# Kernel optimization log

Measured on AMD Instinct MI355X. Metric: run time of the kernel, lower is better.

## Reference

```python
import jax, jax.numpy as jnp
import numpy as np
import math

L, D, H, FF, V, S = 6, 512, 8, 2048, 32000, 1024
DH = D // H
EPS = 1e-5

def _ln(x, w, b):
    mu = jnp.mean(x, -1, keepdims=True)
    var = jnp.mean(jnp.square(x - mu), -1, keepdims=True)
    return (x - mu) * jax.lax.rsqrt(var + EPS) * w + b

def setup_inputs() -> dict:
    key = jax.random.key(0)
    ks = jax.random.split(key, 32)
    s = 0.02
    inp = {
        'x': jax.random.randint(ks[0], (4, S), 0, V, dtype=jnp.int32),
        'mask': jnp.ones((4, S), dtype=jnp.int32),
        'emb': jax.random.normal(ks[1], (V, D), jnp.float32) * s,
        'pos': jax.random.normal(ks[2], (S, D), jnp.float32) * s,
        'Wq': jax.random.normal(ks[3], (L, D, D), jnp.float32) * s,
        'bq': jnp.zeros((L, D), jnp.float32),
        'Wk': jax.random.normal(ks[4], (L, D, D), jnp.float32) * s,
        'bk': jnp.zeros((L, D), jnp.float32),
        'Wv': jax.random.normal(ks[5], (L, D, D), jnp.float32) * s,
        'bv': jnp.zeros((L, D), jnp.float32),
        'Wo': jax.random.normal(ks[6], (L, D, D), jnp.float32) * s,
        'bo': jnp.zeros((L, D), jnp.float32),
        'rel_bias': jax.random.normal(ks[7], (L, 2 * S - 1, H), jnp.float32) * s,
        'scale': jnp.full((L,), math.sqrt(DH), jnp.float32),
        'n1w': jnp.ones((L, D), jnp.float32), 'n1b': jnp.zeros((L, D), jnp.float32),
        'n2w': jnp.ones((L, D), jnp.float32), 'n2b': jnp.zeros((L, D), jnp.float32),
        'f1w': jax.random.normal(ks[8], (L, D, FF), jnp.float32) * s,
        'f1b': jnp.zeros((L, FF), jnp.float32),
        'f2w': jax.random.normal(ks[9], (L, FF, D), jnp.float32) * s,
        'f2b': jnp.zeros((L, D), jnp.float32),
        'fnw': jnp.ones((D,), jnp.float32), 'fnb': jnp.zeros((D,), jnp.float32),
        'fcw': jax.random.normal(ks[10], (D, V), jnp.float32) * s,
        'fcb': jnp.zeros((V,), jnp.float32),
    }
    return inp

def reference(x, mask, emb, pos, Wq, bq, Wk, bk, Wv, bv, Wo, bo, rel_bias, scale,
              n1w, n1b, n2w, n2b, f1w, f1b, f2w, f2b, fnw, fnb, fcw, fcb):
    B, seq = x.shape
    h = emb[x] * jnp.float32(math.sqrt(D)) + pos[None, :seq, :]
    # relative position index table: j - i + seq - 1, values in [0, 2*seq-2]
    r = jnp.arange(seq)
    rp = r[None, :] - r[:, None] + seq - 1  # (S, S)
    # pairwise valid mask (b,1,S,S)
    m2 = (mask[:, None, None, :] * mask[:, None, :, None]) != 0
    for l in range(L):
        q = (h @ Wq[l] + bq[l]).reshape(B, seq, H, DH)
        k = (h @ Wk[l] + bk[l]).reshape(B, seq, H, DH)
        v = (h @ Wv[l] + bv[l]).reshape(B, seq, H, DH)
        scores = jnp.einsum('bihd,bjhd->bhij', q, k) / scale[l]
        bias = rel_bias[l][rp]                      # (S,S,H)
        scores = scores + jnp.transpose(bias, (2, 0, 1))[None]
        scores = jnp.where(m2, scores, -jnp.inf)    # masked_fill(mask==0, -inf)
        attn = jnp.einsum('bhij,bjhd->bihd', scores, v).reshape(B, seq, D)
        attn = attn @ Wo[l] + bo[l]
        h = _ln(h + attn, n1w[l], n1b[l])
        ff = jax.nn.gelu(h @ f1w[l] + f1b[l], approximate=False) @ f2w[l] + f2b[l]
        h = _ln(h + ff, n2w[l], n2b[l])
    h = _ln(h, fnw, fnb)
    return h @ fcw + fcb
```

## Files before the change

### kernel.cpp

```cpp
#include <hip/hip_runtime.h>
#include <cmath>

#define S_LEN  1024
#define DMODEL 512
#define NHEAD  8
#define DHEAD  64
#define FFDIM  2048
#define VOCAB  32000
#define NLAYER 6
#define BATCHN 4
#define ROWS   (BATCHN * S_LEN)

typedef float    f32x4 __attribute__((ext_vector_type(4)));
typedef _Float16 f16x4 __attribute__((ext_vector_type(4)));
typedef _Float16 f16x8 __attribute__((ext_vector_type(8)));

__device__ __forceinline__ void glds16(const _Float16* g, _Float16* l) {
    __builtin_amdgcn_global_load_lds(
        (const __attribute__((address_space(1))) void*)g,
        (__attribute__((address_space(3))) void*)l, 16, 0, 0);
}

template<int MT, int NT, int EPI, int OUT16>
__global__ __launch_bounds__(256)
void hgemm_k(const _Float16* __restrict__ A, long lda,
             const _Float16* __restrict__ Bt, long ldb,
             void* __restrict__ Cg, long ldc, int K,
             const float* __restrict__ bias)
{
    constexpr int BMt = 32 * MT, BNt = 32 * NT;
    constexpr int ASZ = BMt * 64, BSZ = BNt * 64;
    __shared__ _Float16 As[2 * ASZ];
    __shared__ _Float16 Bs[2 * BSZ];

    const int t = threadIdx.x, w = t >> 6, lane = t & 63;
    const int m0 = blockIdx.x * BMt, n0 = blockIdx.y * BNt;
    const int lr = lane & 15, hk = lane >> 4;
    const int rsw = lr & 7;
    const int swz = ((lane & 7) ^ (lane >> 3)) * 8;

    const _Float16* Ab = A  + (long)(m0 + w * 8 * MT + (lane >> 3)) * lda + swz;
    const _Float16* Bb = Bt + (long)(n0 + w * 8 * NT + (lane >> 3)) * ldb + swz;

    f32x4 acc[MT][NT];
#pragma unroll
    for (int i = 0; i < MT; i++)
#pragma unroll
        for (int j = 0; j < NT; j++) acc[i][j] = f32x4{0.f, 0.f, 0.f, 0.f};

    const int wrow = (w >> 1) * 16 * MT;
    const int wcol = (w & 1) * 16 * NT;

    auto stage = [&](int buf, int kt) {
#pragma unroll
        for (int i = 0; i < MT; i++)
            glds16(Ab + (long)i * 8 * lda + kt, &As[buf * ASZ + (w * 8 * MT + i * 8) * 64]);
#pragma unroll
        for (int i = 0; i < NT; i++)
            glds16(Bb + (long)i * 8 * ldb + kt, &Bs[buf * BSZ + (w * 8 * NT + i * 8) * 64]);
    };

    stage(0, 0);
    __syncthreads();
    int cur = 0;
    for (int kt = 0; kt < K; kt += 64) {
        if (kt + 64 < K) stage(cur ^ 1, kt + 64);
#pragma unroll
        for (int kc = 0; kc < 64; kc += 32) {
            const int coff = ((((kc >> 3) + hk) ^ rsw) << 3);
            f16x8 af[MT], bf[NT];
#pragma unroll
            for (int mi = 0; mi < MT; mi++)
                af[mi] = *(const f16x8*)&As[cur * ASZ + (wrow + mi * 16 + lr) * 64 + coff];
#pragma unroll
            for (int ni = 0; ni < NT; ni++)
                bf[ni] = *(const f16x8*)&Bs[cur * BSZ + (wcol + ni * 16 + lr) * 64 + coff];
#pragma unroll
            for (int mi = 0; mi < MT; mi++)
#pragma unroll
                for (int ni = 0; ni < NT; ni++)
                    acc[mi][ni] = __builtin_amdgcn_mfma_f32_16x16x32_f16(af[mi], bf[ni], acc[mi][ni], 0, 0, 0);
        }
        __syncthreads();
        cur ^= 1;
    }

    const int crow = (lane >> 4) * 4, ccol = lane & 15;
#pragma unroll
    for (int mi = 0; mi < MT; mi++)
#pragma unroll
        for (int ni = 0; ni < NT; ni++)
#pragma unroll
            for (int q = 0; q < 4; q++) {
                int gm = m0 + wrow + mi * 16 + crow + q;
                int gn = n0 + wcol + ni * 16 + ccol;
                float v = acc[mi][ni][q];
                if (bias) v += bias[gn];
                if (EPI == 2) v = 0.5f * v * (1.0f + erff(v * 0.70710678118654752f));
                long ci = (long)gm * ldc + gn;
                if (OUT16) ((_Float16*)Cg)[ci] = (_Float16)v;
                else       ((float*)Cg)[ci] = v;
            }
}

__global__ __launch_bounds__(256)
void ktv_k(const _Float16* __restrict__ kt, const _Float16* __restrict__ vt,
           _Float16* __restrict__ M, const float* __restrict__ scale_p)
{
    const int z = blockIdx.x;
    const int wave = threadIdx.x >> 6, lane = threadIdx.x & 63;
    const int lr = lane & 15, lk = (lane >> 4) * 8;
    const long base = (long)z * DHEAD * S_LEN;

    f32x4 acc[4];
#pragma unroll
    for (int i = 0; i < 4; i++) acc[i] = f32x4{0.f, 0.f, 0.f, 0.f};

    for (int j = 0; j < S_LEN; j += 32) {
        f16x8 a = *(const f16x8*)&vt[base + (long)(wave * 16 + lr) * S_LEN + j + lk];
#pragma unroll
        for (int ni = 0; ni < 4; ni++) {
            f16x8 b = *(const f16x8*)&kt[base + (long)(ni * 16 + lr) * S_LEN + j + lk];
            acc[ni] = __builtin_amdgcn_mfma_f32_16x16x32_f16(a, b, acc[ni], 0, 0, 0);
        }
    }

    const float inv = 1.0f / scale_p[0];
    const int crow = (lane >> 4) * 4, ccol = lane & 15;
#pragma unroll
    for (int ni = 0; ni < 4; ni++)
#pragma unroll
        for (int q = 0; q < 4; q++) {
            int gm = wave * 16 + crow + q;
            int gn = ni * 16 + ccol;
            M[(long)z * 4096 + (long)gm * 64 + gn] = (_Float16)(acc[ni][q] * inv);
        }
}

__global__ __launch_bounds__(256)
void toep_k(const _Float16* __restrict__ dv,
            const _Float16* __restrict__ vt,
            const _Float16* __restrict__ q,
            const _Float16* __restrict__ M,
            _Float16* __restrict__ ao)
{
    __shared__ _Float16 Qs[64 * 64];
    __shared__ _Float16 Ms[64 * 64];
    __shared__ _Float16 Vs[2][64 * 64];
    __shared__ _Float16 dseg[1088];

    const int t = threadIdx.x, w = t >> 6, lane = t & 63;
    const int z = blockIdx.z, zb = z >> 3, zh = z & 7;
    const int m0 = blockIdx.x * 64;
    const int lr = lane & 15, hk = lane >> 4;
    const int rsw = lr & 7;
    const int swz = ((lane & 7) ^ (lane >> 3)) * 8;
    const int wrow = w * 16;

    const _Float16* qa = q  + (long)(zb * S_LEN + m0 + w * 16 + (lane >> 3)) * 1536 + zh * 64 + swz;
    const _Float16* ma = M  + (long)z * 4096 + (long)(w * 16 + (lane >> 3)) * 64 + swz;
    const _Float16* va = vt + (long)z * (DHEAD * S_LEN) + (long)(w * 16 + (lane >> 3)) * S_LEN + swz;

#pragma unroll
    for (int i = 0; i < 2; i++) glds16(qa + (long)i * 8 * 1536, &Qs[(w * 16 + i * 8) * 64]);
#pragma unroll
    for (int i = 0; i < 2; i++) glds16(ma + i * 8 * 64, &Ms[(w * 16 + i * 8) * 64]);
#pragma unroll
    for (int i = 0; i < 2; i++) glds16(va + (long)i * 8 * S_LEN, &Vs[0][(w * 16 + i * 8) * 64]);
    {
        const _Float16* dp = dv + zh * 2048 + (960 - m0);
        for (int i = t; i < 1088; i += 256) dseg[i] = dp[i];
    }
    __syncthreads();

    f32x4 acc[4];
#pragma unroll
    for (int i = 0; i < 4; i++) acc[i] = f32x4{0.f, 0.f, 0.f, 0.f};

#pragma unroll
    for (int kc = 0; kc < 64; kc += 32) {
        const int coff = ((((kc >> 3) + hk) ^ rsw) << 3);
        f16x8 aq = *(const f16x8*)&Qs[(wrow + lr) * 64 + coff];
#pragma unroll
        for (int ni = 0; ni < 4; ni++) {
            f16x8 bm = *(const f16x8*)&Ms[(ni * 16 + lr) * 64 + coff];
            acc[ni] = __builtin_amdgcn_mfma_f32_16x16x32_f16(aq, bm, acc[ni], 0, 0, 0);
        }
    }

    int cur = 0;
    for (int kt = 0; kt < S_LEN; kt += 64) {
        if (kt + 64 < S_LEN) {
#pragma unroll
            for (int i = 0; i < 2; i++)
                glds16(va + (long)i * 8 * S_LEN + kt + 64, &Vs[cur ^ 1][(w * 16 + i * 8) * 64]);
        }
#pragma unroll
        for (int kc = 0; kc < 64; kc += 32) {
            const int coff = ((((kc >> 3) + hk) ^ rsw) << 3);
            f16x8 at_;
            const int xb = kt + kc + hk * 8 + 63 - wrow - lr;
#pragma unroll
            for (int u = 0; u < 8; u++) at_[u] = dseg[xb + u];
#pragma unroll
            for (int ni = 0; ni < 4; ni++) {
                f16x8 bv_ = *(const f16x8*)&Vs[cur][(ni * 16 + lr) * 64 + coff];
                acc[ni] = __builtin_amdgcn_mfma_f32_16x16x32_f16(at_, bv_, acc[ni], 0, 0, 0);
            }
        }
        __syncthreads();
        cur ^= 1;
    }

    const int crow = (lane >> 4) * 4, ccol = lane & 15;
    const long cbase = (long)zb * (S_LEN * DMODEL) + zh * DHEAD;
#pragma unroll
    for (int ni = 0; ni < 4; ni++)
#pragma unroll
        for (int qq = 0; qq < 4; qq++) {
            int gm = m0 + wrow + crow + qq;
            int gn = ni * 16 + ccol;
            ao[cbase + (long)gm * DMODEL + gn] = (_Float16)acc[ni][qq];
        }
}

__global__ void embed_k(const int* __restrict__ x, const float* __restrict__ emb,
                        const float* __restrict__ pos, float* __restrict__ h,
                        _Float16* __restrict__ h16)
{
    int row = blockIdx.x;
    int s   = row & (S_LEN - 1);
    int tok = x[row];
    int c   = threadIdx.x * 4;
    f32x4 e = *(const f32x4*)(emb + (long)tok * DMODEL + c);
    f32x4 p = *(const f32x4*)(pos + (long)s * DMODEL + c);
    f32x4 o = e * 22.62741699796952f + p;
    *(f32x4*)(h + (long)row * DMODEL + c) = o;
    f16x4 o16;
#pragma unroll
    for (int j = 0; j < 4; j++) o16[j] = (_Float16)o[j];
    *(f16x4*)(h16 + (long)row * DMODEL + c) = o16;
}

__global__ void ln_k(const float* __restrict__ x, const float* __restrict__ add,
                     const float* __restrict__ w, const float* __restrict__ bb,
                     float* __restrict__ out, _Float16* __restrict__ out16)
{
    int row  = blockIdx.x;
    int lane = threadIdx.x;
    const float* xp = x + (long)row * DMODEL + lane * 8;
    f32x4 a = *(const f32x4*)xp;
    f32x4 b4 = *(const f32x4*)(xp + 4);
    if (add) {
        const float* ap = add + (long)row * DMODEL + lane * 8;
        a  += *(const f32x4*)ap;
        b4 += *(const f32x4*)(ap + 4);
    }
    float v[8] = {a[0],a[1],a[2],a[3],b4[0],b4[1],b4[2],b4[3]};
    float s = 0.f;
#pragma unroll
    for (int i = 0; i < 8; i++) s += v[i];
#pragma unroll
    for (int off = 32; off; off >>= 1) s += __shfl_xor(s, off);
    float mu = s * (1.0f / 512.0f);
    float d2 = 0.f;
#pragma unroll
    for (int i = 0; i < 8; i++) { v[i] -= mu; d2 += v[i] * v[i]; }
#pragma unroll
    for (int off = 32; off; off >>= 1) d2 += __shfl_xor(d2, off);
    float r = rsqrtf(d2 * (1.0f / 512.0f) + 1e-5f);
    const float* wp = w  + lane * 8;
    const float* bp = bb + lane * 8;
    float o[8];
#pragma unroll
    for (int i = 0; i < 8; i++) o[i] = v[i] * r * wp[i] + bp[i];
    float* op = out + (long)row * DMODEL + lane * 8;
    *(f32x4*)op       = f32x4{o[0], o[1], o[2], o[3]};
    *(f32x4*)(op + 4) = f32x4{o[4], o[5], o[6], o[7]};
    f16x8 o16;
#pragma unroll
    for (int i = 0; i < 8; i++) o16[i] = (_Float16)o[i];
    *(f16x8*)(out16 + (long)row * DMODEL + lane * 8) = o16;
}

__global__ void wcvt_k(const float* __restrict__ in, _Float16* __restrict__ out,
                       int R, int C, long inZ, long outZ)
{
    __shared__ float tile[32][33];
    int z = blockIdx.z;
    int c0 = blockIdx.x * 32, r0 = blockIdx.y * 32;
    int tx = threadIdx.x, ty = threadIdx.y;
#pragma unroll
    for (int i = 0; i < 4; i++)
        tile[ty + i * 8][tx] = in[(long)z * inZ + (long)(r0 + ty + i * 8) * C + c0 + tx];
    __syncthreads();
#pragma unroll
    for (int i = 0; i < 4; i++)
        out[(long)z * outZ + (long)(c0 + ty + i * 8) * R + r0 + tx] = (_Float16)tile[tx][ty + i * 8];
}

__global__ void tv16_k(const _Float16* __restrict__ v, long ldv, _Float16* __restrict__ vt)
{
    __shared__ _Float16 tile[32][33];
    int z = blockIdx.z;
    int b = z >> 3, hh = z & 7;
    int j0 = blockIdx.x * 32, d0 = blockIdx.y * 32;
    long ibase = (long)b * S_LEN * ldv + hh * DHEAD;
    long obase = (long)z * (DHEAD * S_LEN);
    int tx = threadIdx.x, ty = threadIdx.y;
#pragma unroll
    for (int i = 0; i < 4; i++)
        tile[ty + i * 8][tx] = v[ibase + (long)(j0 + ty + i * 8) * ldv + d0 + tx];
    __syncthreads();
#pragma unroll
    for (int i = 0; i < 4; i++)
        vt[obase + (long)(d0 + ty + i * 8) * S_LEN + j0 + tx] = tile[tx][ty + i * 8];
}

__global__ void bcat_k(const float* __restrict__ bq, const float* __restrict__ bk,
                       const float* __restrict__ bv, float* __restrict__ o)
{
    int l = blockIdx.x, t = threadIdx.x;
    o[l * 1536 + t]        = bq[l * 512 + t];
    o[l * 1536 + 512 + t]  = bk[l * 512 + t];
    o[l * 1536 + 1024 + t] = bv[l * 512 + t];
}

__global__ void dvec_k(const float* __restrict__ rel, _Float16* __restrict__ dv)
{
    int lh = blockIdx.x;
    int l = lh >> 3, hh = lh & 7;
    for (int t = threadIdx.x; t < 2048; t += 256)
        dv[(long)lh * 2048 + t] = (t < 2047) ? (_Float16)rel[(long)l * 2047 * 8 + (long)t * 8 + hh]
                                             : (_Float16)0.0f;
}

extern "C" void kernel_launch(void* const* d_in, const int* in_sizes, int n_in,
                              void* d_out, int out_size, void* d_ws, size_t ws_size,
                              hipStream_t stream)
{
    (void)in_sizes; (void)n_in; (void)out_size; (void)ws_size;

    const int*   x    = (const int*)d_in[0];
    const float* emb  = (const float*)d_in[2];
    const float* pos  = (const float*)d_in[3];
    const float* Wq   = (const float*)d_in[4];
    const float* bq   = (const float*)d_in[5];
    const float* Wk   = (const float*)d_in[6];
    const float* bk   = (const float*)d_in[7];
    const float* Wv   = (const float*)d_in[8];
    const float* bv   = (const float*)d_in[9];
    const float* Wo   = (const float*)d_in[10];
    const float* bo   = (const float*)d_in[11];
    const float* rel  = (const float*)d_in[12];
    const float* scal = (const float*)d_in[13];
    const float* n1w  = (const float*)d_in[14];
    const float* n1b  = (const float*)d_in[15];
    const float* n2w  = (const float*)d_in[16];
    const float* n2b  = (const float*)d_in[17];
    const float* f1w  = (const float*)d_in[18];
    const float* f1b  = (const float*)d_in[19];
    const float* f2w  = (const float*)d_in[20];
    const float* f2b  = (const float*)d_in[21];
    const float* fnw  = (const float*)d_in[22];
    const float* fnb  = (const float*)d_in[23];
    const float* fcw  = (const float*)d_in[24];
    const float* fcb  = (const float*)d_in[25];

    char* ws = (char*)d_ws;
    size_t off = 0;
    auto alloc = [&](size_t bytes) { char* p = ws + off; off += (bytes + 255) & ~(size_t)255; return p; };
    float*    h      = (float*)alloc((size_t)ROWS * DMODEL * 4);
    float*    proj   = (float*)alloc((size_t)ROWS * DMODEL * 4);
    float*    ff2    = (float*)alloc((size_t)ROWS * DMODEL * 4);
    _Float16* h16    = (_Float16*)alloc((size_t)ROWS * DMODEL * 2);
    _Float16* qkv16  = (_Float16*)alloc((size_t)ROWS * 3 * DMODEL * 2);
    _Float16* kt16   = (_Float16*)alloc((size_t)ROWS * DMODEL * 2);
    _Float16* vt16   = (_Float16*)alloc((size_t)ROWS * DMODEL * 2);
    _Float16* ao16   = (_Float16*)alloc((size_t)ROWS * DMODEL * 2);
    _Float16* ff116  = (_Float16*)alloc((size_t)ROWS * FFDIM * 2);
    _Float16* M16    = (_Float16*)alloc((size_t)32 * 4096 * 2);
    _Float16* wqkvT  = (_Float16*)alloc((size_t)NLAYER * 3 * DMODEL * DMODEL * 2);
    _Float16* woT    = (_Float16*)alloc((size_t)NLAYER * DMODEL * DMODEL * 2);
    _Float16* f1T    = (_Float16*)alloc((size_t)NLAYER * DMODEL * FFDIM * 2);
    _Float16* f2T    = (_Float16*)alloc((size_t)NLAYER * DMODEL * FFDIM * 2);
    _Float16* fcT    = (_Float16*)alloc((size_t)VOCAB * DMODEL * 2);
    float*    bqkv   = (float*)alloc((size_t)NLAYER * 3 * DMODEL * 4);
    _Float16* dv16   = (_Float16*)alloc((size_t)NLAYER * NHEAD * 2048 * 2);

    dim3 b256(256), bT(32, 8);

    wcvt_k<<<dim3(16, 16, NLAYER), bT, 0, stream>>>(Wq, wqkvT,               DMODEL, DMODEL, (long)DMODEL*DMODEL, (long)3*DMODEL*DMODEL);
    wcvt_k<<<dim3(16, 16, NLAYER), bT, 0, stream>>>(Wk, wqkvT + 512*512,     DMODEL, DMODEL, (long)DMODEL*DMODEL, (long)3*DMODEL*DMODEL);
    wcvt_k<<<dim3(16, 16, NLAYER), bT, 0, stream>>>(Wv, wqkvT + 2*512*512,   DMODEL, DMODEL, (long)DMODEL*DMODEL, (long)3*DMODEL*DMODEL);
    wcvt_k<<<dim3(16, 16, NLAYER), bT, 0, stream>>>(Wo, woT,                 DMODEL, DMODEL, (long)DMODEL*DMODEL, (long)DMODEL*DMODEL);
    wcvt_k<<<dim3(FFDIM/32, 16, NLAYER), bT, 0, stream>>>(f1w, f1T,          DMODEL, FFDIM,  (long)DMODEL*FFDIM,  (long)DMODEL*FFDIM);
    wcvt_k<<<dim3(16, FFDIM/32, NLAYER), bT, 0, stream>>>(f2w, f2T,          FFDIM,  DMODEL, (long)DMODEL*FFDIM,  (long)DMODEL*FFDIM);
    wcvt_k<<<dim3(VOCAB/32, 16, 1), bT, 0, stream>>>(fcw, fcT,               DMODEL, VOCAB,  0, 0);
    bcat_k<<<NLAYER, 512, 0, stream>>>(bq, bk, bv, bqkv);
    dvec_k<<<NLAYER * NHEAD, 256, 0, stream>>>(rel, dv16);

    embed_k<<<ROWS, 128, 0, stream>>>(x, emb, pos, h, h16);

    for (int l = 0; l < NLAYER; l++) {
        const long lw  = (long)l * DMODEL * DMODEL;
        const long lff = (long)l * DMODEL * FFDIM;

        hgemm_k<2,4,0,1><<<dim3(64, 12), b256, 0, stream>>>(
            h16, DMODEL, wqkvT + l * 3 * 512 * 512, DMODEL,
            qkv16, 3 * DMODEL, DMODEL, bqkv + l * 3 * DMODEL);

        tv16_k<<<dim3(32, 2, 32), bT, 0, stream>>>(qkv16 + 512,  3 * DMODEL, kt16);
        tv16_k<<<dim3(32, 2, 32), bT, 0, stream>>>(qkv16 + 1024, 3 * DMODEL, vt16);

        ktv_k<<<32, b256, 0, stream>>>(kt16, vt16, M16, scal + l);

        toep_k<<<dim3(16, 1, 32), b256, 0, stream>>>(
            dv16 + (long)l * NHEAD * 2048, vt16, qkv16, M16, ao16);

        hgemm_k<2,2,0,0><<<dim3(64, 8), b256, 0, stream>>>(
            ao16, DMODEL, woT + lw, DMODEL, proj, DMODEL, DMODEL, bo + l * DMODEL);

        ln_k<<<ROWS, 64, 0, stream>>>(h, proj, n1w + l * DMODEL, n1b + l * DMODEL, h, h16);

        hgemm_k<2,4,2,1><<<dim3(64, 16), b256, 0, stream>>>(
            h16, DMODEL, f1T + lff, DMODEL, ff116, FFDIM, DMODEL, f1b + l * FFDIM);

        hgemm_k<2,2,0,0><<<dim3(64, 8), b256, 0, stream>>>(
            ff116, FFDIM, f2T + lff, FFDIM, ff2, DMODEL, FFDIM, f2b + l * DMODEL);

        ln_k<<<ROWS, 64, 0, stream>>>(h, ff2, n2w + l * DMODEL, n2b + l * DMODEL, h, h16);
    }

    ln_k<<<ROWS, 64, 0, stream>>>(h, nullptr, fnw, fnb, proj, h16);

    hgemm_k<4,4,0,0><<<dim3(32, VOCAB / 128), b256, 0, stream>>>(
        h16, DMODEL, fcT, DMODEL, (float*)d_out, VOCAB, DMODEL, fcb);
}
```

Measured before the change: 1.335 ms.

## Replace GEMM with triple-buffered pipelined kernel and retune tiles per call

Replaces the double-buffered GEMM with a templated kernel that uses a three-stage LDS ring over 32-wide K slices. It waits on outstanding vector-memory counts so loads for later stages stay in flight during MFMA work, and needs only one barrier per stage. Tile shapes, wave layout and occupancy hints are retuned per call site. The large vocab projection now uses 512-thread blocks with 256x256 tiles and a block-ID swizzle for L2 locality. The gain depends on the hand-written waitcnt counts matching the loads each thread issues, and the larger tiles cut the number of blocks in flight.

```diff
diff --git a/kernel.cpp b/kernel.cpp
--- a/kernel.cpp
+++ b/kernel.cpp
@@ -21,26 +21,46 @@
         (__attribute__((address_space(3))) void*)l, 16, 0, 0);
 }
 
-template<int MT, int NT, int EPI, int OUT16>
-__global__ __launch_bounds__(256)
-void hgemm_k(const _Float16* __restrict__ A, long lda,
+template<int N> __device__ __forceinline__ void waitvm() {
+    if constexpr (N == 0)      asm volatile("s_waitcnt vmcnt(0)" ::: "memory");
+    else if constexpr (N == 3) asm volatile("s_waitcnt vmcnt(3)" ::: "memory");
+    else if constexpr (N == 4) asm volatile("s_waitcnt vmcnt(4)" ::: "memory");
+}
+
+template<int WM, int WN, int MT, int NT, int EPI, int OUT16, int SWZ8, int OCC>
+__global__ __launch_bounds__(WM * WN * 64, OCC)
+void pgemm_k(const _Float16* __restrict__ A, long lda,
              const _Float16* __restrict__ Bt, long ldb,
              void* __restrict__ Cg, long ldc, int K,
              const float* __restrict__ bias)
 {
-    constexpr int BMt = 32 * MT, BNt = 32 * NT;
-    constexpr int ASZ = BMt * 64, BSZ = BNt * 64;
-    __shared__ _Float16 As[2 * ASZ];
-    __shared__ _Float16 Bs[2 * BSZ];
+    constexpr int T   = WM * WN * 64;
+    constexpr int BMt = WM * MT * 16;
+    constexpr int BNt = WN * NT * 16;
+    constexpr int SR  = T / 4;
+    constexpr int RA  = BMt / SR;
+    constexpr int RB  = BNt / SR;
+    constexpr int L   = RA + RB;
+    constexpr int ASZ = BMt * 32, BSZ = BNt * 32;
+
+    __shared__ _Float16 As[3 * ASZ];
+    __shared__ _Float16 Bs[3 * BSZ];
+
+    int bx = blockIdx.x, by = blockIdx.y;
+    if (SWZ8) {
+        int nb  = gridDim.x * gridDim.y;
+        int id  = by * gridDim.x + bx;
+        int id2 = (id & 7) * (nb >> 3) + (id >> 3);
+        bx = id2 % gridDim.x;
+        by = id2 / gridDim.x;
+    }
+    const int m0 = bx * BMt, n0 = by * BNt;
 
     const int t = threadIdx.x, w = t >> 6, lane = t & 63;
-    const int m0 = blockIdx.x * BMt, n0 = blockIdx.y * BNt;
+    const int sub = t >> 2, ch = t & 3;
+    const int wm = w / WN, wn = w % WN;
+    const int wrow = wm * MT * 16, wcol = wn * NT * 16;
     const int lr = lane & 15, hk = lane >> 4;
-    const int rsw = lr & 7;
-    const int swz = ((lane & 7) ^ (lane >> 3)) * 8;
-
-    const _Float16* Ab = A  + (long)(m0 + w * 8 * MT + (lane >> 3)) * lda + swz;
-    const _Float16* Bb = Bt + (long)(n0 + w * 8 * NT + (lane >> 3)) * ldb + swz;
 
     f32x4 acc[MT][NT];
 #pragma unroll
@@ -48,44 +68,55 @@
 #pragma unroll
         for (int j = 0; j < NT; j++) acc[i][j] = f32x4{0.f, 0.f, 0.f, 0.f};
 
-    const int wrow = (w >> 1) * 16 * MT;
-    const int wcol = (w & 1) * 16 * NT;
-
-    auto stage = [&](int buf, int kt) {
-#pragma unroll
-        for (int i = 0; i < MT; i++)
-            glds16(Ab + (long)i * 8 * lda + kt, &As[buf * ASZ + (w * 8 * MT + i * 8) * 64]);
-#pragma unroll
-        for (int i = 0; i < NT; i++)
-            glds16(Bb + (long)i * 8 * ldb + kt, &Bs[buf * BSZ + (w * 8 * NT + i * 8) * 64]);
+    const int nst = K >> 5;
+
+    auto stage = [&](int tt) {
+        const int kt = tt << 5;
+        _Float16* Ad = &As[(tt % 3) * ASZ];
+        _Float16* Bd = &Bs[(tt % 3) * BSZ];
+#pragma unroll
+        for (int i = 0; i < RA; i++) {
+            int lrow = i * SR + sub;
+            glds16(A + (long)(m0 + lrow) * lda + kt + ((ch ^ ((lrow >> 1) & 3)) << 3),
+                   Ad + (i * SR + w * 16) * 32);
+        }
+#pragma unroll
+        for (int i = 0; i < RB; i++) {
+            int lrow = i * SR + sub;
+            glds16(Bt + (long)(n0 + lrow) * ldb + kt + ((ch ^ ((lrow >> 1) & 3)) << 3),
+                   Bd + (i * SR + w * 16) * 32);
+        }
     };
 
-    stage(0, 0);
-    __syncthreads();
-    int cur = 0;
-    for (int kt = 0; kt < K; kt += 64) {
-        if (kt + 64 < K) stage(cur ^ 1, kt + 64);
-#pragma unroll
-        for (int kc = 0; kc < 64; kc += 32) {
-            const int coff = ((((kc >> 3) + hk) ^ rsw) << 3);
-            f16x8 af[MT], bf[NT];
-#pragma unroll
-            for (int mi = 0; mi < MT; mi++)
-                af[mi] = *(const f16x8*)&As[cur * ASZ + (wrow + mi * 16 + lr) * 64 + coff];
+    stage(0);
+    stage(1);
+
+    for (int tt = 0; tt < nst; ++tt) {
+        if (tt < nst - 1) waitvm<L>(); else waitvm<0>();
+        asm volatile("s_barrier" ::: "memory");
+        if (tt + 2 < nst) stage(tt + 2);
+
+        const _Float16* Ar = &As[(tt % 3) * ASZ];
+        const _Float16* Br = &Bs[(tt % 3) * BSZ];
+        f16x8 af[MT], bf[NT];
+#pragma unroll
+        for (int mi = 0; mi < MT; mi++) {
+            int r = wrow + mi * 16 + lr;
+            af[mi] = *(const f16x8*)&Ar[r * 32 + ((hk ^ ((r >> 1) & 3)) << 3)];
+        }
+#pragma unroll
+        for (int ni = 0; ni < NT; ni++) {
+            int r = wcol + ni * 16 + lr;
+            bf[ni] = *(const f16x8*)&Br[r * 32 + ((hk ^ ((r >> 1) & 3)) << 3)];
+        }
+#pragma unroll
+        for (int mi = 0; mi < MT; mi++)
 #pragma unroll
             for (int ni = 0; ni < NT; ni++)
-                bf[ni] = *(const f16x8*)&Bs[cur * BSZ + (wcol + ni * 16 + lr) * 64 + coff];
-#pragma unroll
-            for (int mi = 0; mi < MT; mi++)
-#pragma unroll
-                for (int ni = 0; ni < NT; ni++)
-                    acc[mi][ni] = __builtin_amdgcn_mfma_f32_16x16x32_f16(af[mi], bf[ni], acc[mi][ni], 0, 0, 0);
-        }
-        __syncthreads();
-        cur ^= 1;
-    }
-
-    const int crow = (lane >> 4) * 4, ccol = lane & 15;
+                acc[mi][ni] = __builtin_amdgcn_mfma_f32_16x16x32_f16(af[mi], bf[ni], acc[mi][ni], 0, 0, 0);
+    }
+
+    const int crow = hk * 4, ccol = lr;
 #pragma unroll
     for (int mi = 0; mi < MT; mi++)
 #pragma unroll
@@ -388,7 +419,7 @@
     float*    bqkv   = (float*)alloc((size_t)NLAYER * 3 * DMODEL * 4);
     _Float16* dv16   = (_Float16*)alloc((size_t)NLAYER * NHEAD * 2048 * 2);
 
-    dim3 b256(256), bT(32, 8);
+    dim3 bT(32, 8);
 
     wcvt_k<<<dim3(16, 16, NLAYER), bT, 0, stream>>>(Wq, wqkvT,               DMODEL, DMODEL, (long)DMODEL*DMODEL, (long)3*DMODEL*DMODEL);
     wcvt_k<<<dim3(16, 16, NLAYER), bT, 0, stream>>>(Wk, wqkvT + 512*512,     DMODEL, DMODEL, (long)DMODEL*DMODEL, (long)3*DMODEL*DMODEL);
@@ -406,27 +437,27 @@
         const long lw  = (long)l * DMODEL * DMODEL;
         const long lff = (long)l * DMODEL * FFDIM;
 
-        hgemm_k<2,4,0,1><<<dim3(64, 12), b256, 0, stream>>>(
+        pgemm_k<2,2,4,4,0,1,0,3><<<dim3(32, 12), 256, 0, stream>>>(
             h16, DMODEL, wqkvT + l * 3 * 512 * 512, DMODEL,
             qkv16, 3 * DMODEL, DMODEL, bqkv + l * 3 * DMODEL);
 
         tv16_k<<<dim3(32, 2, 32), bT, 0, stream>>>(qkv16 + 512,  3 * DMODEL, kt16);
         tv16_k<<<dim3(32, 2, 32), bT, 0, stream>>>(qkv16 + 1024, 3 * DMODEL, vt16);
 
-        ktv_k<<<32, b256, 0, stream>>>(kt16, vt16, M16, scal + l);
-
-        toep_k<<<dim3(16, 1, 32), b256, 0, stream>>>(
+        ktv_k<<<32, 256, 0, stream>>>(kt16, vt16, M16, scal + l);
+
+        toep_k<<<dim3(16, 1, 32), 256, 0, stream>>>(
             dv16 + (long)l * NHEAD * 2048, vt16, qkv16, M16, ao16);
 
-        hgemm_k<2,2,0,0><<<dim3(64, 8), b256, 0, stream>>>(
+        pgemm_k<1,4,4,2,0,0,0,4><<<dim3(64, 4), 256, 0, stream>>>(
             ao16, DMODEL, woT + lw, DMODEL, proj, DMODEL, DMODEL, bo + l * DMODEL);
 
         ln_k<<<ROWS, 64, 0, stream>>>(h, proj, n1w + l * DMODEL, n1b + l * DMODEL, h, h16);
 
-        hgemm_k<2,4,2,1><<<dim3(64, 16), b256, 0, stream>>>(
+        pgemm_k<2,2,4,4,2,1,0,3><<<dim3(32, 16), 256, 0, stream>>>(
             h16, DMODEL, f1T + lff, DMODEL, ff116, FFDIM, DMODEL, f1b + l * FFDIM);
 
-        hgemm_k<2,2,0,0><<<dim3(64, 8), b256, 0, stream>>>(
+        pgemm_k<1,4,4,2,0,0,0,4><<<dim3(64, 4), 256, 0, stream>>>(
             ff116, FFDIM, f2T + lff, FFDIM, ff2, DMODEL, FFDIM, f2b + l * DMODEL);
 
         ln_k<<<ROWS, 64, 0, stream>>>(h, ff2, n2w + l * DMODEL, n2b + l * DMODEL, h, h16);
@@ -434,6 +465,6 @@
 
     ln_k<<<ROWS, 64, 0, stream>>>(h, nullptr, fnw, fnb, proj, h16);
 
-    hgemm_k<4,4,0,0><<<dim3(32, VOCAB / 128), b256, 0, stream>>>(
+    pgemm_k<2,4,8,4,0,0,1,2><<<dim3(16, VOCAB / 256), 512, 0, stream>>>(
         h16, DMODEL, fcT, DMODEL, (float*)d_out, VOCAB, DMODEL, fcb);
 }
```

Result: slower. 1.391 ms (+4.2%).
